# Optimization experiments

Hardware: AMD Instinct MI355X
Metric: run time of the kernel (lower is better)

The kernel has to match this reference:

```python
import jax, jax.numpy as jnp
import numpy as np

NEG = -1e9  # large negative for masked logits (TRT uses dtype min)

def _rotate_every_two(x):
    # pairs (x0,x1) -> (-x1, x0), interleaved along last dim
    xr = x.reshape(*x.shape[:-1], -1, 2)
    rot = jnp.stack([-xr[..., 1], xr[..., 0]], axis=-1)
    return rot.reshape(x.shape)

def _apply_rope(x, cos, sin):
    # rot_dim == cos.shape[-1]; here it equals the full inner dim
    rot_dim = cos.shape[-1]
    x_rot, x_pass = x[..., :rot_dim], x[..., rot_dim:]
    x_rot = x_rot * cos + _rotate_every_two(x_rot) * sin
    return jnp.concatenate([x_rot, x_pass], axis=-1) if x_pass.shape[-1] else x_rot

def setup_inputs() -> dict:
    key = jax.random.key(0)
    ks = jax.random.split(key, 12)
    B, N, D_MODEL, H, DH = 2, 2048, 1024, 16, 64
    INNER = H * DH
    x = jax.random.normal(ks[0], (B, N, D_MODEL), dtype=jnp.float32)
    # rope angles: build realistic cos/sin tables repeated per head
    pos = jnp.arange(N, dtype=jnp.float32)
    inv = 1.0 / (10000.0 ** (jnp.arange(0, DH, 2, dtype=jnp.float32) / DH))
    ang = pos[:, None] * inv[None, :]              # [N, DH/2]
    ang = jnp.repeat(ang, 2, axis=-1)              # [N, DH] interleaved pairs
    ang = jnp.tile(ang, (1, H))                    # [N, INNER]
    rope_cos = jnp.broadcast_to(jnp.cos(ang)[None], (B, N, INNER)).astype(jnp.float32)
    rope_sin = jnp.broadcast_to(jnp.sin(ang)[None], (B, N, INNER)).astype(jnp.float32)
    input_lengths = jax.random.randint(ks[1], (B,), N // 2, N + 1, dtype=jnp.int32)
    s = 1.0 / np.sqrt(D_MODEL)
    Wq = jax.random.normal(ks[2], (D_MODEL, INNER), dtype=jnp.float32) * s
    bq = jnp.zeros((INNER,), jnp.float32)
    Wk = jax.random.normal(ks[3], (D_MODEL, INNER), dtype=jnp.float32) * s
    bk = jnp.zeros((INNER,), jnp.float32)
    Wv = jax.random.normal(ks[4], (D_MODEL, INNER), dtype=jnp.float32) * s
    bv = jnp.zeros((INNER,), jnp.float32)
    Wo = jax.random.normal(ks[5], (INNER, D_MODEL), dtype=jnp.float32) * (1.0 / np.sqrt(INNER))
    bo = jnp.zeros((D_MODEL,), jnp.float32)
    return {"x": x, "rope_cos": rope_cos, "rope_sin": rope_sin,
            "input_lengths": input_lengths,
            "Wq": Wq, "bq": bq, "Wk": Wk, "bk": bk, "Wv": Wv, "bv": bv,
            "Wo": Wo, "bo": bo}

def reference(x, rope_cos, rope_sin, input_lengths, Wq, bq, Wk, bk, Wv, bv, Wo, bo):
    B, N, _ = x.shape
    H, DH = 16, 64
    q = x @ Wq + bq
    k = x @ Wk + bk
    v = x @ Wv + bv
    q = _apply_rope(q, rope_cos, rope_sin)
    k = _apply_rope(k, rope_cos, rope_sin)
    # split heads: [B,N,H,DH] -> [B,H,N,DH]
    q = q.reshape(B, N, H, DH).transpose(0, 2, 1, 3)
    k = k.reshape(B, N, H, DH).transpose(0, 2, 1, 3)
    v = v.reshape(B, N, H, DH).transpose(0, 2, 1, 3)
    # NOTE: faithful to the non-plugin source path, q is NOT pre-scaled
    scores = jnp.einsum('bhqd,bhkd->bhqk', q, k)
    key_mask = jnp.arange(N)[None, :] < input_lengths[:, None]  # [B,N]
    scores = scores + jnp.where(key_mask, 0.0, NEG).astype(scores.dtype)[:, None, None, :]
    probs = jax.nn.softmax(scores, axis=-1)
    ctx = jnp.einsum('bhqk,bhkd->bhqd', probs, v)  # [B,H,N,DH]
    ctx = ctx.transpose(0, 2, 1, 3).reshape(B, N, H * DH)
    out = ctx @ Wo + bo
    out = out * key_mask[..., None].astype(out.dtype)
    return out
```

## Files before the change

kernel.cpp:

```cpp
#include <hip/hip_runtime.h>
#include <hip/hip_bf16.h>


typedef __fp16 fp16x2 __attribute__((ext_vector_type(2)));
typedef _Float16 f16x8 __attribute__((ext_vector_type(8)));
typedef float f32x4 __attribute__((ext_vector_type(4)));
typedef float f32x16 __attribute__((ext_vector_type(16)));

#define NEGBIG (-1.0e9f)

__device__ inline f32x4 mfma16(f16x8 a, f16x8 b, f32x4 c) {
  return __builtin_amdgcn_mfma_f32_16x16x32_f16(a, b, c, 0, 0, 0);
}
__device__ inline f32x16 mfma32(f16x8 a, f16x8 b, f32x16 c) {
  return __builtin_amdgcn_mfma_f32_32x32x16_f16(a, b, c, 0, 0, 0);
}

__device__ inline void gload16(const void* g, void* l) {
  __builtin_amdgcn_global_load_lds(
      (const __attribute__((address_space(1))) void*)g,
      (__attribute__((address_space(3))) void*)l, 16, 0, 0);
}

__device__ inline unsigned pk2u(float a, float b) {
  union { fp16x2 h; unsigned u; } x;
  x.h = __builtin_amdgcn_cvt_pkrtz(a, b);
  return x.u;
}

__global__ __launch_bounds__(256) void prep_kernel(
    const float* __restrict__ x, const float* __restrict__ Wq,
    const float* __restrict__ Wk, const float* __restrict__ Wv,
    const float* __restrict__ Wo, _Float16* __restrict__ xh,
    _Float16* __restrict__ wt) {
  __shared__ float tile[32][33];
  const int z = blockIdx.z;
  const int tx = threadIdx.x, ty = threadIdx.y;
  if (z == 4) {
    const int bid = blockIdx.y * 32 + blockIdx.x;
    const int t = ty * 32 + tx;
#pragma unroll
    for (int i = 0; i < 4; ++i) {
      const int o = bid * 1024 + i * 256 + t;
      const float4 v = ((const float4*)x)[o];
      union { _Float16 h[4]; short4 s; } u;
      u.h[0] = (_Float16)v.x; u.h[1] = (_Float16)v.y;
      u.h[2] = (_Float16)v.z; u.h[3] = (_Float16)v.w;
      ((short4*)xh)[o] = u.s;
    }
    return;
  }
  const float* W = (z == 0) ? Wq : (z == 1) ? Wk : (z == 2) ? Wv : Wo;
  _Float16* dh = wt + (size_t)z * 1024 * 1024;
  const int j0 = blockIdx.x * 32, k0 = blockIdx.y * 32;
  for (int i = ty; i < 32; i += 8)
    tile[i][tx] = W[(size_t)(k0 + i) * 1024 + j0 + tx];
  __syncthreads();
  for (int i = ty; i < 32; i += 8)
    dh[(size_t)(j0 + i) * 1024 + k0 + tx] = (_Float16)tile[tx][i];
}

template <int TM, int EPI>
__global__ __launch_bounds__(256) void gemm_kernel(
    const _Float16* __restrict__ A, const _Float16* __restrict__ B,
    const float* __restrict__ bias0, const float* __restrict__ bias1,
    const float* __restrict__ bias2,
    const float* __restrict__ ropeC, const float* __restrict__ ropeS,
    const int* __restrict__ lens,
    _Float16* __restrict__ outQK, _Float16* __restrict__ outVT,
    float* __restrict__ outF) {
  constexpr int MI = TM / 32;
  __shared__ __align__(16) _Float16 smem[(TM + 128) * 32];
  const int t = threadIdx.x;
  const int w = t >> 6, lane = t & 63;
  const int wr = w >> 1, wc = w & 1;
  const int fr = lane & 15, fg = lane >> 4;
  const int mtile = blockIdx.x, ntile = blockIdx.y;

  const int srow = t >> 2;
  const int skel = (t & 3) << 3;
  const size_t aBase = (size_t)(mtile * TM + srow) * 1024 + skel;
  const size_t bBase = (size_t)(ntile * 128 + srow) * 1024 + skel;
  const int ldst = t * 8;
  _Float16* lA = &smem[0];
  _Float16* lB = &smem[TM * 32];

  f32x4 acc[MI][4];
#pragma unroll
  for (int i = 0; i < MI; ++i)
#pragma unroll
    for (int j = 0; j < 4; ++j) {
      acc[i][j][0] = 0.f; acc[i][j][1] = 0.f; acc[i][j][2] = 0.f; acc[i][j][3] = 0.f;
    }

  for (int k0 = 0; k0 < 1024; k0 += 32) {
    gload16(A + aBase + k0, lA + ldst);
    if constexpr (TM == 128) gload16(A + aBase + k0 + 64 * 1024, lA + ldst + 2048);
    gload16(B + bBase + k0, lB + ldst);
    gload16(B + bBase + k0 + 64 * 1024, lB + ldst + 2048);
    __syncthreads();

    f16x8 af[MI], bf[4];
#pragma unroll
    for (int mi = 0; mi < MI; ++mi)
      af[mi] = *(const f16x8*)&lA[(wr * (TM / 2) + mi * 16 + fr) * 32 + fg * 8];
#pragma unroll
    for (int ni = 0; ni < 4; ++ni)
      bf[ni] = *(const f16x8*)&lB[(wc * 64 + ni * 16 + fr) * 32 + fg * 8];
#pragma unroll
    for (int mi = 0; mi < MI; ++mi)
#pragma unroll
      for (int ni = 0; ni < 4; ++ni)
        acc[mi][ni] = mfma16(af[mi], bf[ni], acc[mi][ni]);
    __syncthreads();
  }

  const int rowbase = mtile * TM + wr * (TM / 2);
  const int colbase = ntile * 128 + wc * 64;

  if constexpr (EPI == 0) {
    const int which = colbase >> 10;
    if (which < 2) {
      const float* bias = which ? bias1 : bias0;
#pragma unroll
      for (int ni = 0; ni < 4; ++ni) {
        const int gcol = colbase + ni * 16 + fr;
        const int jj = gcol & 1023;
        const int hh = jj >> 6, dd = jj & 63;
        const float bv = bias[jj];
#pragma unroll
        for (int mi = 0; mi < MI; ++mi) {
#pragma unroll
          for (int r = 0; r < 4; ++r) {
            const int grow = rowbase + mi * 16 + fg * 4 + r;
            const int b = grow >> 11, n = grow & 2047;
            float val = acc[mi][ni][r] + bv;
            float part = __shfl_xor(val, 1);
            const size_t ro = (size_t)(b * 2048 + n) * 1024 + jj;
            const float c = ropeC[ro], s = ropeS[ro];
            float rot = (fr & 1) ? (val * c + part * s) : (val * c - part * s);
            if (!which) rot *= 1.44269504f;
            outQK[((size_t)((which * 2 + b) * 16 + hh) * 2048 + n) * 64 + dd] =
                (_Float16)rot;
          }
        }
      }
    } else {
#pragma unroll
      for (int ni = 0; ni < 4; ++ni) {
        const int gcol = colbase + ni * 16 + fr;
        const int jj = gcol & 1023;
        const int hh = jj >> 6, dd = jj & 63;
        const float bv = bias2[jj];
#pragma unroll
        for (int mi = 0; mi < MI; ++mi) {
          const int n0 = rowbase + mi * 16 + fg * 4;
          const int b = n0 >> 11, n = n0 & 2047;
          union { _Float16 h[4]; short4 s4; } u;
#pragma unroll
          for (int r = 0; r < 4; ++r) u.h[r] = (_Float16)(acc[mi][ni][r] + bv);
          *(short4*)(outVT + ((size_t)(b * 16 + hh) * 64 + dd) * 2048 + n) = u.s4;
        }
      }
    }
  } else {
    const int b = rowbase >> 11;
    const int len = lens[b];
#pragma unroll
    for (int ni = 0; ni < 4; ++ni) {
      const int gcol = colbase + ni * 16 + fr;
      const float bv = bias0[gcol];
#pragma unroll
      for (int mi = 0; mi < MI; ++mi) {
#pragma unroll
        for (int r = 0; r < 4; ++r) {
          const int m = rowbase + mi * 16 + fg * 4 + r;
          const int n = m & 2047;
          float val = acc[mi][ni][r] + bv;
          if (n >= len) val = 0.f;
          outF[(size_t)m * 1024 + gcol] = val;
        }
      }
    }
  }
}

__global__ __launch_bounds__(128, 4) void attn_kernel(
    const _Float16* __restrict__ qk, const _Float16* __restrict__ vt,
    const int* __restrict__ lens, float* __restrict__ po,
    float2* __restrict__ ml) {
  __shared__ __align__(16) char lds[16384];
  const int t = threadIdx.x;
  const int w = t >> 6, lane = t & 63;
  const int lq = lane & 31, hi = lane >> 5;
  const int gid = blockIdx.x;
  const int bh_seg = (gid & 7) + ((gid >> 8) << 3);
  const int qtile = (gid >> 3) & 31;
  const int bh = bh_seg >> 1, seg = bh_seg & 1;
  const int b = bh >> 4, h = bh & 15;
  const int len = lens[b];
  const int q0w = qtile * 64 + w * 32;
  const size_t qoff = (size_t)(b * 16 + h) * 2048 * 64;
  const size_t koff = (size_t)((2 + b) * 16 + h) * 2048 * 64;
  const size_t voff = (size_t)(b * 16 + h) * 64 * 2048;

  f16x8 qf[4];
#pragma unroll
  for (int ks = 0; ks < 4; ++ks)
    qf[ks] = *(const f16x8*)(qk + qoff + (size_t)(q0w + lq) * 64 + ks * 16 + hi * 8);

  const int srow = t >> 3;
  const int ss = (t & 7) ^ (srow & 7);
  const size_t kg = koff + (size_t)srow * 64 + ss * 8;
  const int vd = srow + ((ss >> 2) << 5);
  const size_t vg1 = voff + (size_t)vd * 2048 + (ss & 3) * 8;
  const size_t vg2 = voff + (size_t)(vd + 16) * 2048 + (ss & 3) * 8;

  f32x16 o0, o1;
#pragma unroll
  for (int i = 0; i < 16; ++i) { o0[i] = 0.f; o1[i] = 0.f; }
  float mrun = -1e30f, lsum = 0.f;

#define STAGE(bi, kb_) do { \
    char* dst = lds + (bi) * 8192 + t * 16; \
    const size_t k064 = (size_t)(kb_) * 2048;  \
    gload16(qk + kg + k064, dst); \
    gload16(qk + kg + k064 + 1024, dst + 2048); \
    gload16(vt + vg1 + (kb_) * 32, dst + 4096); \
    gload16(vt + vg2 + (kb_) * 32, dst + 6144); \
  } while (0)

  const int nkb = (len + 31) >> 5;
  const int nk0 = (nkb + 1) >> 1;
  const int tb0 = seg ? nk0 : 0;
  const int tb1 = seg ? nkb : nk0;

  STAGE(0, tb0);

  for (int kb = tb0; kb < tb1; ++kb) {
    const int cur = (kb - tb0) & 1;
    if (kb + 1 < tb1) {
      STAGE(cur ^ 1, kb + 1);
      asm volatile("s_waitcnt vmcnt(4)" ::: "memory");
    } else {
      asm volatile("s_waitcnt vmcnt(0)" ::: "memory");
    }
    __builtin_amdgcn_s_barrier();

    const char* Kb = lds + cur * 8192;
    const char* Vb = Kb + 4096;
    const int rsw = (lq & 7) << 4;

    f32x16 s0;
#pragma unroll
    for (int i = 0; i < 16; ++i) s0[i] = 0.f;
    __builtin_amdgcn_s_setprio(1);
#pragma unroll
    for (int ks = 0; ks < 4; ++ks) {
      const f16x8 kf = *(const f16x8*)(Kb + lq * 128 + ((ks * 32 + hi * 16) ^ rsw));
      s0 = mfma32(kf, qf[ks], s0);
    }
    __builtin_amdgcn_s_setprio(0);

    if (kb == nkb - 1 && (len & 31)) {
#pragma unroll
      for (int r = 0; r < 16; ++r) {
        const int key = kb * 32 + (r & 3) + ((r >> 2) << 3) + hi * 4;
        if (key >= len) s0[r] = NEGBIG;
      }
    }

    float mx = s0[0];
#pragma unroll
    for (int r = 1; r < 16; ++r) mx = fmaxf(mx, s0[r]);
    mx = fmaxf(mx, __shfl_xor(mx, 32));

    if (!__all(mx <= mrun + 8.f)) {
      const float mnew = fmaxf(mrun, mx);
      const float scq = exp2f(mrun - mnew);
      mrun = mnew;
      lsum *= scq;
      float sc[16];
#pragma unroll
      for (int r = 0; r < 16; ++r)
        sc[r] = __shfl(scq, (r & 3) + ((r >> 2) << 3) + hi * 4);
#pragma unroll
      for (int r = 0; r < 16; ++r) { o0[r] *= sc[r]; o1[r] *= sc[r]; }
    }

    unsigned W[8];
    float ps = 0.f;
#pragma unroll
    for (int u = 0; u < 4; ++u) {
      const float p0 = exp2f(s0[4 * u + 0] - mrun);
      const float p1 = exp2f(s0[4 * u + 1] - mrun);
      const float p2 = exp2f(s0[4 * u + 2] - mrun);
      const float p3 = exp2f(s0[4 * u + 3] - mrun);
      ps += (p0 + p1) + (p2 + p3);
      W[2 * u] = pk2u(p0, p1);
      W[2 * u + 1] = pk2u(p2, p3);
    }
    ps += __shfl_xor(ps, 32);
    lsum += ps;

    __builtin_amdgcn_s_setprio(1);
#pragma unroll
    for (int ks = 0; ks < 2; ++ks) {
      const unsigned w0 = W[4 * ks + 0], w1 = W[4 * ks + 1];
      const unsigned w2 = W[4 * ks + 2], w3 = W[4 * ks + 3];
      const unsigned sendA = hi ? w0 : w2;
      const unsigned sendB = hi ? w1 : w3;
      const unsigned recvA = __shfl_xor(sendA, 32);
      const unsigned recvB = __shfl_xor(sendB, 32);
      union { unsigned u[4]; f16x8 v; } af;
      af.u[0] = hi ? recvA : w0;
      af.u[1] = hi ? recvB : w1;
      af.u[2] = hi ? w2 : recvA;
      af.u[3] = hi ? w3 : recvB;
      const int g0 = ks * 2 + hi;
      const f16x8 v0f = *(const f16x8*)(Vb + lq * 128 + ((g0 << 4) ^ rsw));
      const f16x8 v1f = *(const f16x8*)(Vb + lq * 128 + (((g0 + 4) << 4) ^ rsw));
      o0 = mfma32(af.v, v0f, o0);
      o1 = mfma32(af.v, v1f, o1);
    }
    __builtin_amdgcn_s_setprio(0);

    asm volatile("" ::: "memory");
    __builtin_amdgcn_s_barrier();
  }
#undef STAGE

  const size_t rowbase = (size_t)bh * 2048 + q0w;
  float* pod = po + ((size_t)seg * 65536 + rowbase) * 64;
#pragma unroll
  for (int r = 0; r < 16; ++r) {
    const int qr = (r & 3) + ((r >> 2) << 3) + hi * 4;
    pod[qr * 64 + lq] = o0[r];
    pod[qr * 64 + 32 + lq] = o1[r];
  }
  if (hi == 0) {
    float2 v; v.x = mrun; v.y = lsum;
    ml[(size_t)seg * 65536 + rowbase + lq] = v;
  }
}

__global__ __launch_bounds__(256) void combine_kernel(
    const float* __restrict__ po, const float2* __restrict__ ml,
    _Float16* __restrict__ ctx) {
  const int tid = blockIdx.x * 256 + threadIdx.x;
  const int row = tid >> 2, dg = tid & 3;
  const float2 a = ml[row], c = ml[65536 + row];
  const float m = fmaxf(a.x, c.x);
  const float e0 = exp2f(a.x - m), e1 = exp2f(c.x - m);
  const float inv = 1.f / (a.y * e0 + c.y * e1);
  const float f0 = e0 * inv, f1 = e1 * inv;
  const float4* p0 = (const float4*)(po + (size_t)row * 64 + dg * 16);
  const float4* p1 = (const float4*)(po + (size_t)(65536 + row) * 64 + dg * 16);
  const int bh = row >> 11, n = row & 2047, b = bh >> 4, h = bh & 15;
  _Float16* dst = ctx + ((size_t)(b * 2048 + n) * 1024 + h * 64 + dg * 16);
#pragma unroll
  for (int i = 0; i < 4; ++i) {
    const float4 v0 = p0[i], v1 = p1[i];
    union { _Float16 h[4]; short4 s4; } u;
    u.h[0] = (_Float16)(v0.x * f0 + v1.x * f1);
    u.h[1] = (_Float16)(v0.y * f0 + v1.y * f1);
    u.h[2] = (_Float16)(v0.z * f0 + v1.z * f1);
    u.h[3] = (_Float16)(v0.w * f0 + v1.w * f1);
    *(short4*)(dst + i * 4) = u.s4;
  }
}


extern "C" void kernel_launch(void* const* d_in, const int* in_sizes, int n_in,
                              void* d_out, int out_size, void* d_ws, size_t ws_size,
                              hipStream_t stream) {
  const float* x = (const float*)d_in[0];
  const float* rc = (const float*)d_in[1];
  const float* rs = (const float*)d_in[2];
  const int* lens = (const int*)d_in[3];
  const float* Wq = (const float*)d_in[4];
  const float* bq = (const float*)d_in[5];
  const float* Wk = (const float*)d_in[6];
  const float* bk = (const float*)d_in[7];
  const float* Wv = (const float*)d_in[8];
  const float* bv = (const float*)d_in[9];
  const float* Wo = (const float*)d_in[10];
  const float* bo = (const float*)d_in[11];
  float* out = (float*)d_out;

  char* ws = (char*)d_ws;
  const size_t MB = 1024 * 1024;
  _Float16* XH = (_Float16*)(ws + 0);
  _Float16* WT = (_Float16*)(ws + 8 * MB);
  _Float16* QK = (_Float16*)(ws + 16 * MB);
  _Float16* VT = (_Float16*)(ws + 32 * MB);
  _Float16* CTX = (_Float16*)(ws + 40 * MB);
  float* PO = (float*)(ws + 48 * MB);
  float2* ML = (float2*)(ws + 81 * MB);

  prep_kernel<<<dim3(32, 32, 5), dim3(32, 8), 0, stream>>>(x, Wq, Wk, Wv, Wo,
                                                           XH, WT);
  gemm_kernel<128, 0><<<dim3(32, 24), 256, 0, stream>>>(
      XH, WT, bq, bk, bv, rc, rs, nullptr, QK, VT, nullptr);
  attn_kernel<<<2048, 128, 0, stream>>>(QK, VT, lens, PO, ML);
  combine_kernel<<<1024, 256, 0, stream>>>(PO, ML, CTX);
  gemm_kernel<64, 2><<<dim3(64, 8), 256, 0, stream>>>(
      CTX, WT + (size_t)3 * 1024 * 1024, bo, nullptr, nullptr, nullptr,
      nullptr, lens, nullptr, nullptr, out);
}
```

Baseline: 161.2 us.

## Split attention keys four ways with 4-wave blocks and fp16 partial outputs

Attention blocks grow from 2 to 4 waves sharing each staged K/V tile, which halves per-thread global-to-LDS loads. The key range is split into four segments instead of two. Partial outputs are normalized per segment and stored as packed fp16, and the combine kernel merges four segments. The softmax inner loop folds the running-max subtraction into the MFMA accumulator init, uses v_max3 and a packed fp16 dot for the row sum, and calls raw exp2 intrinsics. The trade-off is more partial-result traffic and combine work from four segments, and some precision loss from storing fp16 partials.

```diff
diff --git a/kernel.cpp b/kernel.cpp
--- a/kernel.cpp
+++ b/kernel.cpp
@@ -26,6 +26,12 @@
   union { fp16x2 h; unsigned u; } x;
   x.h = __builtin_amdgcn_cvt_pkrtz(a, b);
   return x.u;
+}
+
+__device__ inline float max3f(float a, float b, float c) {
+  float d;
+  asm("v_max3_f32 %0, %1, %2, %3" : "=v"(d) : "v"(a), "v"(b), "v"(c));
+  return d;
 }
 
 __global__ __launch_bounds__(256) void prep_kernel(
@@ -185,21 +191,22 @@
   }
 }
 
-__global__ __launch_bounds__(128, 4) void attn_kernel(
+__global__ __launch_bounds__(256, 8) void attn_kernel(
     const _Float16* __restrict__ qk, const _Float16* __restrict__ vt,
-    const int* __restrict__ lens, float* __restrict__ po,
+    const int* __restrict__ lens, unsigned* __restrict__ po,
     float2* __restrict__ ml) {
   __shared__ __align__(16) char lds[16384];
   const int t = threadIdx.x;
   const int w = t >> 6, lane = t & 63;
   const int lq = lane & 31, hi = lane >> 5;
   const int gid = blockIdx.x;
-  const int bh_seg = (gid & 7) + ((gid >> 8) << 3);
-  const int qtile = (gid >> 3) & 31;
-  const int bh = bh_seg >> 1, seg = bh_seg & 1;
+  const int xcd = gid & 7, idx = gid >> 3;
+  const int qtile = idx & 15;
+  const int c = ((idx >> 4) << 3) + xcd;
+  const int bh = c >> 2, seg = c & 3;
   const int b = bh >> 4, h = bh & 15;
   const int len = lens[b];
-  const int q0w = qtile * 64 + w * 32;
+  const int q0w = qtile * 128 + w * 32;
   const size_t qoff = (size_t)(b * 16 + h) * 2048 * 64;
   const size_t koff = (size_t)((2 + b) * 16 + h) * 2048 * 64;
   const size_t voff = (size_t)(b * 16 + h) * 64 * 2048;
@@ -213,27 +220,25 @@
   const int ss = (t & 7) ^ (srow & 7);
   const size_t kg = koff + (size_t)srow * 64 + ss * 8;
   const int vd = srow + ((ss >> 2) << 5);
-  const size_t vg1 = voff + (size_t)vd * 2048 + (ss & 3) * 8;
-  const size_t vg2 = voff + (size_t)(vd + 16) * 2048 + (ss & 3) * 8;
+  const size_t vg = voff + (size_t)vd * 2048 + (ss & 3) * 8;
 
   f32x16 o0, o1;
 #pragma unroll
   for (int i = 0; i < 16; ++i) { o0[i] = 0.f; o1[i] = 0.f; }
-  float mrun = -1e30f, lsum = 0.f;
+  float mrun = 0.f, lsum = 0.f;
+
+  fp16x2 ones2;
+  ones2[0] = (__fp16)1.0f; ones2[1] = (__fp16)1.0f;
 
 #define STAGE(bi, kb_) do { \
     char* dst = lds + (bi) * 8192 + t * 16; \
-    const size_t k064 = (size_t)(kb_) * 2048;  \
-    gload16(qk + kg + k064, dst); \
-    gload16(qk + kg + k064 + 1024, dst + 2048); \
-    gload16(vt + vg1 + (kb_) * 32, dst + 4096); \
-    gload16(vt + vg2 + (kb_) * 32, dst + 6144); \
+    gload16(qk + kg + (size_t)(kb_) * 2048, dst); \
+    gload16(vt + vg + (kb_) * 32, dst + 4096); \
   } while (0)
 
   const int nkb = (len + 31) >> 5;
-  const int nk0 = (nkb + 1) >> 1;
-  const int tb0 = seg ? nk0 : 0;
-  const int tb1 = seg ? nkb : nk0;
+  const int tb0 = (nkb * seg) >> 2;
+  const int tb1 = (nkb * (seg + 1)) >> 2;
 
   STAGE(0, tb0);
 
@@ -241,7 +246,7 @@
     const int cur = (kb - tb0) & 1;
     if (kb + 1 < tb1) {
       STAGE(cur ^ 1, kb + 1);
-      asm volatile("s_waitcnt vmcnt(4)" ::: "memory");
+      asm volatile("s_waitcnt vmcnt(2)" ::: "memory");
     } else {
       asm volatile("s_waitcnt vmcnt(0)" ::: "memory");
     }
@@ -252,8 +257,9 @@
     const int rsw = (lq & 7) << 4;
 
     f32x16 s0;
-#pragma unroll
-    for (int i = 0; i < 16; ++i) s0[i] = 0.f;
+    const float nm = -mrun;
+#pragma unroll
+    for (int i = 0; i < 16; ++i) s0[i] = nm;
     __builtin_amdgcn_s_setprio(1);
 #pragma unroll
     for (int ks = 0; ks < 4; ++ks) {
@@ -270,15 +276,19 @@
       }
     }
 
-    float mx = s0[0];
-#pragma unroll
-    for (int r = 1; r < 16; ++r) mx = fmaxf(mx, s0[r]);
+    const float m0 = max3f(s0[0], s0[1], s0[2]);
+    const float m1 = max3f(s0[3], s0[4], s0[5]);
+    const float m2 = max3f(s0[6], s0[7], s0[8]);
+    const float m3 = max3f(s0[9], s0[10], s0[11]);
+    const float m4 = max3f(s0[12], s0[13], s0[14]);
+    float mx = fmaxf(max3f(m0, m1, m2), max3f(m3, m4, s0[15]));
     mx = fmaxf(mx, __shfl_xor(mx, 32));
 
-    if (!__all(mx <= mrun + 8.f)) {
-      const float mnew = fmaxf(mrun, mx);
-      const float scq = exp2f(mrun - mnew);
-      mrun = mnew;
+    const bool first = (kb == tb0);
+    if (first || !__all(mx <= 8.f)) {
+      const float delta = first ? mx : fmaxf(mx, 0.f);
+      const float scq = __builtin_amdgcn_exp2f(-delta);
+      mrun += delta;
       lsum *= scq;
       float sc[16];
 #pragma unroll
@@ -286,19 +296,25 @@
         sc[r] = __shfl(scq, (r & 3) + ((r >> 2) << 3) + hi * 4);
 #pragma unroll
       for (int r = 0; r < 16; ++r) { o0[r] *= sc[r]; o1[r] *= sc[r]; }
+#pragma unroll
+      for (int i = 0; i < 16; ++i) s0[i] -= delta;
     }
 
     unsigned W[8];
-    float ps = 0.f;
 #pragma unroll
     for (int u = 0; u < 4; ++u) {
-      const float p0 = exp2f(s0[4 * u + 0] - mrun);
-      const float p1 = exp2f(s0[4 * u + 1] - mrun);
-      const float p2 = exp2f(s0[4 * u + 2] - mrun);
-      const float p3 = exp2f(s0[4 * u + 3] - mrun);
-      ps += (p0 + p1) + (p2 + p3);
+      const float p0 = __builtin_amdgcn_exp2f(s0[4 * u + 0]);
+      const float p1 = __builtin_amdgcn_exp2f(s0[4 * u + 1]);
+      const float p2 = __builtin_amdgcn_exp2f(s0[4 * u + 2]);
+      const float p3 = __builtin_amdgcn_exp2f(s0[4 * u + 3]);
       W[2 * u] = pk2u(p0, p1);
       W[2 * u + 1] = pk2u(p2, p3);
+    }
+    float ps = 0.f;
+#pragma unroll
+    for (int i = 0; i < 8; ++i) {
+      union { unsigned u; fp16x2 h; } x; x.u = W[i];
+      ps = __builtin_amdgcn_fdot2(x.h, ones2, ps, false);
     }
     ps += __shfl_xor(ps, 32);
     lsum += ps;
@@ -331,12 +347,13 @@
 #undef STAGE
 
   const size_t rowbase = (size_t)bh * 2048 + q0w;
-  float* pod = po + ((size_t)seg * 65536 + rowbase) * 64;
+  const float li = 1.f / lsum;
+  unsigned* pod = po + ((size_t)seg * 65536 + rowbase) * 32;
 #pragma unroll
   for (int r = 0; r < 16; ++r) {
     const int qr = (r & 3) + ((r >> 2) << 3) + hi * 4;
-    pod[qr * 64 + lq] = o0[r];
-    pod[qr * 64 + 32 + lq] = o1[r];
+    const float lr = __shfl(li, qr);
+    pod[qr * 32 + lq] = pk2u(o0[r] * lr, o1[r] * lr);
   }
   if (hi == 0) {
     float2 v; v.x = mrun; v.y = lsum;
@@ -345,29 +362,33 @@
 }
 
 __global__ __launch_bounds__(256) void combine_kernel(
-    const float* __restrict__ po, const float2* __restrict__ ml,
+    const unsigned* __restrict__ po, const float2* __restrict__ ml,
     _Float16* __restrict__ ctx) {
   const int tid = blockIdx.x * 256 + threadIdx.x;
-  const int row = tid >> 2, dg = tid & 3;
-  const float2 a = ml[row], c = ml[65536 + row];
-  const float m = fmaxf(a.x, c.x);
-  const float e0 = exp2f(a.x - m), e1 = exp2f(c.x - m);
-  const float inv = 1.f / (a.y * e0 + c.y * e1);
-  const float f0 = e0 * inv, f1 = e1 * inv;
-  const float4* p0 = (const float4*)(po + (size_t)row * 64 + dg * 16);
-  const float4* p1 = (const float4*)(po + (size_t)(65536 + row) * 64 + dg * 16);
+  const int row = tid >> 5, dg = tid & 31;
+  const float2 a0 = ml[row];
+  const float2 a1 = ml[65536 + row];
+  const float2 a2 = ml[131072 + row];
+  const float2 a3 = ml[196608 + row];
+  const float m = fmaxf(fmaxf(a0.x, a1.x), fmaxf(a2.x, a3.x));
+  const float w0 = a0.y * __builtin_amdgcn_exp2f(a0.x - m);
+  const float w1 = a1.y * __builtin_amdgcn_exp2f(a1.x - m);
+  const float w2 = a2.y * __builtin_amdgcn_exp2f(a2.x - m);
+  const float w3 = a3.y * __builtin_amdgcn_exp2f(a3.x - m);
+  const float inv = 1.f / (w0 + w1 + w2 + w3);
+  float acc0 = 0.f, acc1 = 0.f;
+  const float f[4] = {w0 * inv, w1 * inv, w2 * inv, w3 * inv};
+#pragma unroll
+  for (int s = 0; s < 4; ++s) {
+    union { unsigned u; fp16x2 h; } x;
+    x.u = po[((size_t)s * 65536 + row) * 32 + dg];
+    acc0 += f[s] * (float)x.h[0];
+    acc1 += f[s] * (float)x.h[1];
+  }
   const int bh = row >> 11, n = row & 2047, b = bh >> 4, h = bh & 15;
-  _Float16* dst = ctx + ((size_t)(b * 2048 + n) * 1024 + h * 64 + dg * 16);
-#pragma unroll
-  for (int i = 0; i < 4; ++i) {
-    const float4 v0 = p0[i], v1 = p1[i];
-    union { _Float16 h[4]; short4 s4; } u;
-    u.h[0] = (_Float16)(v0.x * f0 + v1.x * f1);
-    u.h[1] = (_Float16)(v0.y * f0 + v1.y * f1);
-    u.h[2] = (_Float16)(v0.z * f0 + v1.z * f1);
-    u.h[3] = (_Float16)(v0.w * f0 + v1.w * f1);
-    *(short4*)(dst + i * 4) = u.s4;
-  }
+  _Float16* dst = ctx + ((size_t)(b * 2048 + n) * 1024 + h * 64);
+  dst[dg] = (_Float16)acc0;
+  dst[dg + 32] = (_Float16)acc1;
 }
 
 
@@ -395,15 +416,15 @@
   _Float16* QK = (_Float16*)(ws + 16 * MB);
   _Float16* VT = (_Float16*)(ws + 32 * MB);
   _Float16* CTX = (_Float16*)(ws + 40 * MB);
-  float* PO = (float*)(ws + 48 * MB);
-  float2* ML = (float2*)(ws + 81 * MB);
+  unsigned* PO = (unsigned*)(ws + 48 * MB);
+  float2* ML = (float2*)(ws + 80 * MB);
 
   prep_kernel<<<dim3(32, 32, 5), dim3(32, 8), 0, stream>>>(x, Wq, Wk, Wv, Wo,
                                                            XH, WT);
   gemm_kernel<128, 0><<<dim3(32, 24), 256, 0, stream>>>(
       XH, WT, bq, bk, bv, rc, rs, nullptr, QK, VT, nullptr);
-  attn_kernel<<<2048, 128, 0, stream>>>(QK, VT, lens, PO, ML);
-  combine_kernel<<<1024, 256, 0, stream>>>(PO, ML, CTX);
+  attn_kernel<<<2048, 256, 0, stream>>>(QK, VT, lens, PO, ML);
+  combine_kernel<<<8192, 256, 0, stream>>>(PO, ML, CTX);
   gemm_kernel<64, 2><<<dim3(64, 8), 256, 0, stream>>>(
       CTX, WT + (size_t)3 * 1024 * 1024, bo, nullptr, nullptr, nullptr,
       nullptr, lens, nullptr, nullptr, out);
```

New measurement: 232.2 us. +44.0%, slower.
